# Optimization experiments

Hardware: AMD Instinct MI355X
Metric: run time of the kernel (lower is better)

Reference implementation:

```python
import jax, jax.numpy as jnp
import numpy as np

VOCAB = 32000
HID = 1024
LAYERS = 6
HEADS = 8 * 2  # 16
HEAD_DIM = HID // HEADS
INTER = int(HID * 8 / 3)  # 2730, matches torch int(hidden*8/3)
MAX_POS = 2048
EPS = 1e-5


def setup_inputs() -> dict:
    key = jax.random.key(0)
    ks = jax.random.split(key, 16)
    B, S = 2, 1024
    input_ids = jax.random.randint(ks[0], (B, S), 0, VOCAB)

    def lin(k, out_d, in_d, stack=True):
        shape = (LAYERS, out_d, in_d) if stack else (out_d, in_d)
        return jax.random.normal(k, shape, jnp.float32) * (in_d ** -0.5)

    return {
        "input_ids": input_ids,
        "tok_emb": jax.random.normal(ks[1], (VOCAB, HID), jnp.float32) * 0.02,
        "pos_emb": jax.random.normal(ks[2], (MAX_POS, HID), jnp.float32) * 0.02,
        "qkv_w": lin(ks[3], 3 * HID, HID),
        "o_w": lin(ks[4], HID, HID),
        "gate_w": lin(ks[5], INTER, HID),
        "up_w": lin(ks[6], INTER, HID),
        "down_w": lin(ks[7], HID, INTER),
        "ln1_w": jnp.ones((LAYERS, HID), jnp.float32),
        "ln1_b": jnp.zeros((LAYERS, HID), jnp.float32),
        "ln2_w": jnp.ones((LAYERS, HID), jnp.float32),
        "ln2_b": jnp.zeros((LAYERS, HID), jnp.float32),
        "lnf_w": jnp.ones((HID,), jnp.float32),
        "lnf_b": jnp.zeros((HID,), jnp.float32),
        "head_w": lin(ks[8], VOCAB, HID, stack=False),
    }


def _layernorm(x, w, b):
    mu = jnp.mean(x, axis=-1, keepdims=True)
    var = jnp.mean(jnp.square(x - mu), axis=-1, keepdims=True)
    return (x - mu) * jax.lax.rsqrt(var + EPS) * w + b


def _forward(input_ids, tok_emb, pos_emb, qkv_w, o_w, gate_w, up_w, down_w,
             ln1_w, ln1_b, ln2_w, ln2_b, lnf_w, lnf_b, head_w):
    B, S = input_ids.shape
    h = tok_emb[input_ids] + pos_emb[jnp.arange(S)][None, :, :]  # [B,S,H]
    scale = HEAD_DIM ** -0.5

    def layer(h, p):
        qkv_w, o_w, gate_w, up_w, down_w, l1w, l1b, l2w, l2b = p
        # attention block
        x = _layernorm(h, l1w, l1b)
        qkv = jnp.einsum('bsh,oh->bso', x, qkv_w)  # [B,S,3H]
        qkv = qkv.reshape(B, S, 3, HEADS, HEAD_DIM)
        q, k, v = qkv[:, :, 0], qkv[:, :, 1], qkv[:, :, 2]  # [B,S,Hn,Dh]
        attn = jnp.einsum('bqnd,bknd->bnqk', q, k) * scale  # [B,Hn,S,S]
        attn = jax.nn.softmax(attn, axis=-1)
        ctx = jnp.einsum('bnqk,bknd->bqnd', attn, v).reshape(B, S, HID)
        h = h + jnp.einsum('bsh,oh->bso', ctx, o_w)
        # MLP block (SwiGLU)
        x = _layernorm(h, l2w, l2b)
        gate = jax.nn.silu(jnp.einsum('bsh,ih->bsi', x, gate_w))
        up = jnp.einsum('bsh,ih->bsi', x, up_w)
        h = h + jnp.einsum('bsi,hi->bsh', gate * up, down_w)
        return h, None

    h, _ = jax.lax.scan(layer, h, (qkv_w, o_w, gate_w, up_w, down_w,
                                   ln1_w, ln1_b, ln2_w, ln2_b))
    h = _layernorm(h, lnf_w, lnf_b)
    logits = jnp.einsum('bsh,vh->bsv', h, head_w)  # [B,S,V]
    return logits


def reference(input_ids, tok_emb, pos_emb, qkv_w, o_w, gate_w, up_w, down_w,
              ln1_w, ln1_b, ln2_w, ln2_b, lnf_w, lnf_b, head_w):
    return _forward(input_ids, tok_emb, pos_emb, qkv_w, o_w, gate_w, up_w,
                    down_w, ln1_w, ln1_b, ln2_w, ln2_b, lnf_w, lnf_b, head_w)
```

## Files before the change

### kernel.cpp

```cpp
#include <hip/hip_runtime.h>

typedef unsigned short u16;
typedef __attribute__((ext_vector_type(8))) short bf16x8;
typedef __attribute__((ext_vector_type(8))) unsigned short us8;
typedef __attribute__((ext_vector_type(4))) unsigned short us4;
typedef __attribute__((ext_vector_type(4))) float f32x4;

#define SEQ    1024
#define TOK    2048
#define HID    1024
#define NLAYER 6
#define NHEAD  16
#define HDIM   64
#define QKV3   3072
#define INTER  2730
#define IPAD   2816
#define VOCAB  32000
#define LN_EPS 1e-5f

__device__ __forceinline__ u16 f2bf(float f) {
  unsigned u = __float_as_uint(f);
  return (u16)((u + 0x7fffu + ((u >> 16) & 1u)) >> 16);
}
__device__ __forceinline__ float bf2f(u16 u) {
  return __uint_as_float(((unsigned)u) << 16);
}

__device__ __forceinline__ void gl_lds16(const void* g, void* l) {
  __builtin_amdgcn_global_load_lds(
      (const __attribute__((address_space(1))) void*)g,
      (__attribute__((address_space(3))) void*)l, 16, 0, 0);
}

__global__ __launch_bounds__(256) void embed_kernel(
    const int* __restrict__ ids, const float* __restrict__ tok,
    const float* __restrict__ pos, float* __restrict__ h)
{
  int t = blockIdx.x;
  int s = t & (SEQ - 1);
  int id = ids[t];
  int c = threadIdx.x * 4;
  float4 tv = *(const float4*)(tok + (long)id * HID + c);
  float4 pv = *(const float4*)(pos + (long)s * HID + c);
  float4 o;
  o.x = tv.x + pv.x; o.y = tv.y + pv.y; o.z = tv.z + pv.z; o.w = tv.w + pv.w;
  *(float4*)(h + (long)t * HID + c) = o;
}

__device__ __forceinline__ void ln_body(
    int t, int tid, const float* __restrict__ h, const float* __restrict__ w,
    const float* __restrict__ b, u16* __restrict__ out, float* r1, float* r2)
{
  int lane = tid & 63, wid = tid >> 6;
  float4 v = *(const float4*)(h + (long)t * HID + tid * 4);
  float s1 = v.x + v.y + v.z + v.w;
  float s2 = v.x * v.x + v.y * v.y + v.z * v.z + v.w * v.w;
#pragma unroll
  for (int o = 32; o > 0; o >>= 1) { s1 += __shfl_down(s1, o); s2 += __shfl_down(s2, o); }
  if (lane == 0) { r1[wid] = s1; r2[wid] = s2; }
  __syncthreads();
  float t1 = r1[0] + r1[1] + r1[2] + r1[3];
  float t2 = r2[0] + r2[1] + r2[2] + r2[3];
  float mu = t1 * (1.f / HID);
  float var = t2 * (1.f / HID) - mu * mu;
  float rs = rsqrtf(var + LN_EPS);
  float4 wv = *(const float4*)(w + tid * 4);
  float4 bv = *(const float4*)(b + tid * 4);
  us4 o4;
  o4[0] = f2bf((v.x - mu) * rs * wv.x + bv.x);
  o4[1] = f2bf((v.y - mu) * rs * wv.y + bv.y);
  o4[2] = f2bf((v.z - mu) * rs * wv.z + bv.z);
  o4[3] = f2bf((v.w - mu) * rs * wv.w + bv.w);
  *(us4*)(out + (long)t * HID + tid * 4) = o4;
}

__global__ __launch_bounds__(256) void ln_kernel(
    const float* __restrict__ h, const float* __restrict__ w,
    const float* __restrict__ b, u16* __restrict__ out)
{
  __shared__ float r1[4], r2[4];
  ln_body(blockIdx.x, threadIdx.x, h, w, b, out, r1, r2);
}

__global__ __launch_bounds__(256) void pre_kernel(
    const float* __restrict__ h, const float* __restrict__ lw,
    const float* __restrict__ lb, u16* __restrict__ x,
    const float* __restrict__ qkv_w, const float* __restrict__ o_w,
    const float* __restrict__ gate, const float* __restrict__ up,
    const float* __restrict__ down,
    u16* __restrict__ wq, u16* __restrict__ wo,
    u16* __restrict__ wgu, u16* __restrict__ wd)
{
  __shared__ float r1[4], r2[4];
  int bid = blockIdx.x;
  if (bid < 2048) {
    ln_body(bid, threadIdx.x, h, lw, lb, x, r1, r2);
    return;
  }
  long i = (long)(bid - 2048) * 256 + threadIdx.x;
  us8 o;
  if (i < 393216L) {
    const float* s = qkv_w + i * 8;
#pragma unroll
    for (int j = 0; j < 8; ++j) o[j] = f2bf(s[j]);
    *(us8*)(wq + i * 8) = o;
  } else if (i < 524288L) {
    long i2 = i - 393216L;
    const float* s = o_w + i2 * 8;
#pragma unroll
    for (int j = 0; j < 8; ++j) o[j] = f2bf(s[j]);
    *(us8*)(wo + i2 * 8) = o;
  } else if (i < 1245184L) {
    long i3 = i - 524288L;
    int n = (int)(i3 >> 7);
    int kc = (int)(i3 & 127);
    int g = n >> 1;
    const float* s = (n & 1) ? up : gate;
#pragma unroll
    for (int j = 0; j < 8; ++j) {
      int k = kc * 8 + j;
      o[j] = f2bf((g < INTER) ? s[(long)g * HID + k] : 0.f);
    }
    *(us8*)(wgu + i3 * 8) = o;
  } else {
    long i4 = i - 1245184L;
    int n = (int)(i4 / 352);
    int kc = (int)(i4 % 352);
#pragma unroll
    for (int j = 0; j < 8; ++j) {
      int k = kc * 8 + j;
      o[j] = f2bf((k < INTER) ? down[(long)n * INTER + k] : 0.f);
    }
    *(us8*)(wd + i4 * 8) = o;
  }
}

__global__ __launch_bounds__(256) void fin_kernel(
    const float* __restrict__ h, const float* __restrict__ lw,
    const float* __restrict__ lb, u16* __restrict__ x,
    const float* __restrict__ head_w, u16* __restrict__ whead)
{
  __shared__ float r1[4], r2[4];
  int bid = blockIdx.x;
  if (bid < 2048) {
    ln_body(bid, threadIdx.x, h, lw, lb, x, r1, r2);
    return;
  }
  long i = (long)(bid - 2048) * 256 + threadIdx.x;
  const float* s = head_w + i * 8;
  us8 o;
#pragma unroll
  for (int j = 0; j < 8; ++j) o[j] = f2bf(s[j]);
  *(us8*)(whead + i * 8) = o;
}

__global__ __launch_bounds__(256, 3) void attn_kernel(
    const u16* __restrict__ qkv, const u16* __restrict__ vT,
    u16* __restrict__ ctx)
{
  __shared__ u16 Ks[8][128][8];
  __shared__ u16 Vs[16][64][8];
  __shared__ u16 Ps[4][16 * 128];

  const int tid  = threadIdx.x;
  const int lane = tid & 63;
  const int w    = tid >> 6;
  const int lo   = lane & 15;
  const int hi   = lane >> 4;

  const int z  = blockIdx.x & 31;
  const int qt = blockIdx.x >> 5;
  const int b  = z >> 4, h = z & 15;

  const u16* Qb  = qkv + (long)b * SEQ * QKV3 + h * 64;
  const u16* Kb  = Qb + 1024;
  const u16* Vtb = vT + (long)z * 65536;

  bf16x8 q[2];
#pragma unroll
  for (int ks = 0; ks < 2; ++ks)
    q[ks] = *(const bf16x8*)(Qb + (long)(qt * 64 + w * 16 + lo) * QKV3 + ks * 32 + hi * 8);

  f32x4 po[4];
  float m_run[4], l_run[4];
#pragma unroll
  for (int r = 0; r < 4; ++r) { m_run[r] = -1e30f; l_run[r] = 0.f; }
#pragma unroll
  for (int nd = 0; nd < 4; ++nd) po[nd] = (f32x4){0.f, 0.f, 0.f, 0.f};

  char* Pw = (char*)&Ps[w][0];

  for (int c = 0; c < 8; ++c) {
#pragma unroll
    for (int i = 0; i < 4; ++i) {
      int u = w * 4 + i, g = u & 7, rg = u >> 3;
      gl_lds16(Kb + (long)(c * 128 + rg * 64 + lane) * QKV3 + g * 8, &Ks[g][rg * 64][0]);
    }
#pragma unroll
    for (int i = 0; i < 4; ++i) {
      int kg = w * 4 + i;
      gl_lds16(Vtb + (long)lane * 1024 + c * 128 + kg * 8, &Vs[kg][0][0]);
    }
    __syncthreads();

    f32x4 s[8];
#pragma unroll
    for (int jf = 0; jf < 8; ++jf) s[jf] = (f32x4){0.f, 0.f, 0.f, 0.f};
#pragma unroll
    for (int jf = 0; jf < 8; ++jf) {
      bf16x8 bk[2];
#pragma unroll
      for (int ks = 0; ks < 2; ++ks)
        bk[ks] = *(const bf16x8*)&Ks[ks * 4 + hi][jf * 16 + lo][0];
#pragma unroll
      for (int ks = 0; ks < 2; ++ks)
        s[jf] = __builtin_amdgcn_mfma_f32_16x16x32_bf16(q[ks], bk[ks], s[jf], 0, 0, 0);
    }

    float scf[4];
#pragma unroll
    for (int r = 0; r < 4; ++r) {
      float rm = -1e30f;
#pragma unroll
      for (int jf = 0; jf < 8; ++jf) {
        s[jf][r] *= 0.125f;
        rm = fmaxf(rm, s[jf][r]);
      }
#pragma unroll
      for (int o = 1; o < 16; o <<= 1) rm = fmaxf(rm, __shfl_xor(rm, o));
      float mn = fmaxf(m_run[r], rm);
      float sc = __expf(m_run[r] - mn);
      float rs = 0.f;
#pragma unroll
      for (int jf = 0; jf < 8; ++jf) {
        float e = __expf(s[jf][r] - mn);
        s[jf][r] = e;
        rs += e;
      }
#pragma unroll
      for (int o = 1; o < 16; o <<= 1) rs += __shfl_xor(rs, o);
      l_run[r] = l_run[r] * sc + rs;
      m_run[r] = mn;
      scf[r] = sc;
    }

#pragma unroll
    for (int jf = 0; jf < 8; ++jf)
#pragma unroll
      for (int r = 0; r < 4; ++r) {
        int row = hi * 4 + r;
        int byo = row * 256 + ((((jf * 16 + lo) * 2)) ^ ((row & 7) << 4));
        *(u16*)(Pw + byo) = f2bf(s[jf][r]);
      }
#pragma unroll
    for (int nd = 0; nd < 4; ++nd)
#pragma unroll
      for (int r = 0; r < 4; ++r) po[nd][r] *= scf[r];

    bf16x8 pa[4];
#pragma unroll
    for (int ks2 = 0; ks2 < 4; ++ks2) {
      int row = lo;
      int byo = row * 256 + (((ks2 * 32 + hi * 8) * 2) ^ ((row & 7) << 4));
      pa[ks2] = *(const bf16x8*)(Pw + byo);
    }
#pragma unroll
    for (int nd = 0; nd < 4; ++nd) {
      bf16x8 bv[4];
#pragma unroll
      for (int ks2 = 0; ks2 < 4; ++ks2)
        bv[ks2] = *(const bf16x8*)&Vs[ks2 * 4 + hi][nd * 16 + lo][0];
#pragma unroll
      for (int ks2 = 0; ks2 < 4; ++ks2)
        po[nd] = __builtin_amdgcn_mfma_f32_16x16x32_bf16(pa[ks2], bv[ks2], po[nd], 0, 0, 0);
    }
    __syncthreads();
  }

#pragma unroll
  for (int r = 0; r < 4; ++r) {
    float inv = 1.f / l_run[r];
    int qrow = qt * 64 + w * 16 + hi * 4 + r;
    u16* dst = ctx + (long)(b * SEQ + qrow) * HID + h * 64;
#pragma unroll
    for (int nd = 0; nd < 4; ++nd)
      dst[nd * 16 + lo] = f2bf(po[nd][r] * inv);
  }
}

template<int BM, int BN, int EPI>
__global__ __launch_bounds__(256) void gemm_bt(
    const u16* __restrict__ A, const u16* __restrict__ B,
    void* __restrict__ Cv, const float* __restrict__ resid,
    int lda, int ldb, int ldc, int K, float scale, int bdiv,
    long sA1, long sA2, long sB1, long sB2, long sC1, long sC2)
{
  constexpr int FM = BM / 32;
  constexpr int FN = BN / 32;
  constexpr int TRW = 136;
  constexpr int SMEMU = (EPI == 4 && 128 * TRW > 2 * (BM + BN) * 32)
                        ? 128 * TRW : 2 * (BM + BN) * 32;
  __shared__ u16 smem[SMEMU];
  auto absb = [&](int buf) { return smem + buf * (BM * 32); };
  auto bsb  = [&](int buf) { return smem + 2 * (BM * 32) + buf * (BN * 32); };

  const int tid = threadIdx.x;
  const int lane = tid & 63;
  const int wid = tid >> 6;
  const int wm = wid >> 1, wn = wid & 1;

  const int z = blockIdx.z;
  const long offA = (long)(z / bdiv) * sA1 + (long)(z % bdiv) * sA2;
  const long offB = (long)(z / bdiv) * sB1 + (long)(z % bdiv) * sB2;
  const long offC = (long)(z / bdiv) * sC1 + (long)(z % bdiv) * sC2;

  const u16* Ab = A + offA + (long)blockIdx.x * BM * lda;
  const u16* Bb = B + offB + (long)blockIdx.y * BN * ldb;

  auto stage = [&](int buf, int kt) {
    const u16* a = Ab + (long)kt * 32;
    const u16* bsrc = Bb + (long)kt * 32;
#pragma unroll
    for (int i = 0; i < BM / 64; ++i) {
      int row = i * 64 + wid * 16 + (lane >> 2);
      gl_lds16(a + (long)row * lda + (lane & 3) * 8, absb(buf) + i * 2048 + wid * 512);
    }
#pragma unroll
    for (int i = 0; i < BN / 64; ++i) {
      int row = i * 64 + wid * 16 + (lane >> 2);
      gl_lds16(bsrc + (long)row * ldb + (lane & 3) * 8, bsb(buf) + i * 2048 + wid * 512);
    }
  };

  f32x4 acc[FM][FN];
#pragma unroll
  for (int i = 0; i < FM; ++i)
#pragma unroll
    for (int j = 0; j < FN; ++j) acc[i][j] = (f32x4){0.f, 0.f, 0.f, 0.f};

  int aoff[FM], boff[FN];
#pragma unroll
  for (int i = 0; i < FM; ++i)
    aoff[i] = (wm * (BM / 2) + i * 16 + (lane & 15)) * 32 + (lane >> 4) * 8;
#pragma unroll
  for (int j = 0; j < FN; ++j)
    boff[j] = (wn * (BN / 2) + j * 16 + (lane & 15)) * 32 + (lane >> 4) * 8;

  const int KT = K >> 5;
  stage(0, 0);
  __syncthreads();
  int cur = 0;
  for (int kt = 0; kt < KT; ++kt) {
    if (kt + 1 < KT) stage(cur ^ 1, kt + 1);
    bf16x8 av[FM], bv[FN];
#pragma unroll
    for (int i = 0; i < FM; ++i) av[i] = *(const bf16x8*)(absb(cur) + aoff[i]);
#pragma unroll
    for (int j = 0; j < FN; ++j) bv[j] = *(const bf16x8*)(bsb(cur) + boff[j]);
#pragma unroll
    for (int i = 0; i < FM; ++i)
#pragma unroll
      for (int j = 0; j < FN; ++j)
        acc[i][j] = __builtin_amdgcn_mfma_f32_16x16x32_bf16(av[i], bv[j], acc[i][j], 0, 0, 0);
    __syncthreads();
    cur ^= 1;
  }

  const int r0 = blockIdx.x * BM + wm * (BM / 2) + (lane >> 4) * 4;
  const int c0 = blockIdx.y * BN + wn * (BN / 2) + (lane & 15);

  if (EPI == 4 && blockIdx.y >= 16) {
    u16* Tr = smem;
    const int clb = wn * 64 + (lane & 15);
    const int rlb = wm * 64 + (lane >> 4) * 4;
#pragma unroll
    for (int i = 0; i < FM; ++i) {
#pragma unroll
      for (int j = 0; j < FN; ++j) {
        us4 t4;
#pragma unroll
        for (int r = 0; r < 4; ++r) t4[r] = f2bf(acc[i][j][r]);
        *(us4*)(Tr + (clb + j * 16) * TRW + rlb + i * 16) = t4;
      }
    }
    __syncthreads();
    const int bb  = blockIdx.x >> 3;
    const int k0  = (blockIdx.x & 7) * 128;
    const int vcb = blockIdx.y * 128 - 2048;
    const int c_loc = tid >> 1, half = tid & 1;
    const int vcol = vcb + c_loc;
    u16* vTo = (u16*)(void*)resid;
    u16* dst = vTo + (long)(bb * 16 + (vcol >> 6)) * 65536
             + (long)(vcol & 63) * 1024 + k0 + half * 64;
    const u16* srcl = Tr + c_loc * TRW + half * 64;
#pragma unroll
    for (int j = 0; j < 8; ++j)
      *(us8*)(dst + j * 8) = *(const us8*)(srcl + j * 8);
    return;
  }

#pragma unroll
  for (int i = 0; i < FM; ++i) {
#pragma unroll
    for (int j = 0; j < FN; ++j) {
      f32x4 v = acc[i][j];
#pragma unroll
      for (int r = 0; r < 4; ++r) {
        if (EPI == 3) {
          float pv = __shfl_xor(v[r], 1);
          if ((lane & 1) == 0) {
            float gf = v[r];
            float res = gf / (1.f + __expf(-gf)) * pv;
            int cc = c0 + j * 16;
            long idx = offC + (long)(r0 + i * 16 + r) * ldc + (cc >> 1);
            ((u16*)Cv)[idx] = f2bf(res);
          }
        } else {
          long idx = offC + (long)(r0 + i * 16 + r) * ldc + (c0 + j * 16);
          if (EPI == 0 || EPI == 4) ((u16*)Cv)[idx] = f2bf(v[r] * scale);
          else if (EPI == 1)        ((float*)Cv)[idx] = v[r] * scale;
          else                      ((float*)Cv)[idx] = resid[idx] + v[r];
        }
      }
    }
  }
}

template<int EPI>
__global__ __launch_bounds__(512, 1) void gemm256(
    const u16* __restrict__ A, const u16* __restrict__ B,
    void* __restrict__ Cv, int NB, int ldc)
{
  __shared__ u16 lds[2][2][2][8][128][8];

  const int tid  = threadIdx.x;
  const int lane = tid & 63;
  const int w    = tid >> 6;
  const int wm   = w >> 2;
  const int wn   = w & 3;
  const int arow = lane & 15;
  const int kg   = lane >> 4;

  const int flat = blockIdx.x;
  const int swz  = (flat & 7) * NB + (flat >> 3);
  const int bm   = swz & 7;
  const int bn   = swz >> 3;

  const u16* Ab = A + (long)bm * 256 * 1024;
  const u16* Bb = B + (long)bn * 256 * 1024;

  auto stage = [&](int mat, int d, int half, int t) {
#pragma unroll
    for (int i = 0; i < 2; ++i) {
      const int u  = w * 2 + i;
      const int g  = u & 7;
      const int rg = u >> 3;
      const u16* src = (mat == 0 ? Ab : Bb)
                     + (long)(half * 128 + rg * 64 + lane) * 1024 + t * 64 + g * 8;
      gl_lds16(src, &lds[d][mat][half][g][rg * 64][0]);
    }
  };

  f32x4 acc[2][2][4][2];
#pragma unroll
  for (int qm = 0; qm < 2; ++qm)
#pragma unroll
    for (int qn = 0; qn < 2; ++qn)
#pragma unroll
      for (int f = 0; f < 4; ++f)
#pragma unroll
        for (int n = 0; n < 2; ++n) acc[qm][qn][f][n] = (f32x4){0.f, 0.f, 0.f, 0.f};

  bf16x8 a[4][2];
  bf16x8 b[2][2][2];

  auto rdA = [&](int d, int qm) {
#pragma unroll
    for (int f = 0; f < 4; ++f)
#pragma unroll
      for (int ks = 0; ks < 2; ++ks)
        a[f][ks] = *(const bf16x8*)&lds[d][0][wm][ks * 4 + kg][qm * 64 + f * 16 + arow][0];
  };
  auto rdB = [&](int d, int qn) {
#pragma unroll
    for (int n = 0; n < 2; ++n)
#pragma unroll
      for (int ks = 0; ks < 2; ++ks)
        b[qn][n][ks] = *(const bf16x8*)&lds[d][1][wn >> 1][ks * 4 + kg]
                                          [(wn & 1) * 64 + qn * 32 + n * 16 + arow][0];
  };
  auto mm = [&](int qm, int qn) {
#pragma unroll
    for (int f = 0; f < 4; ++f)
#pragma unroll
      for (int n = 0; n < 2; ++n)
#pragma unroll
        for (int ks = 0; ks < 2; ++ks)
          acc[qm][qn][f][n] = __builtin_amdgcn_mfma_f32_16x16x32_bf16(
              a[f][ks], b[qn][n][ks], acc[qm][qn][f][n], 0, 0, 0);
  };

#define BAR asm volatile("s_barrier" ::: "memory")
#define PRIO1 __builtin_amdgcn_s_setprio(1)
#define PRIO0 __builtin_amdgcn_s_setprio(0)

  stage(1, 0, 0, 0);
  stage(0, 0, 0, 0);
  stage(0, 0, 1, 0);
  stage(1, 0, 1, 0);
  stage(1, 1, 0, 1);
  stage(0, 1, 0, 1);
  asm volatile("s_waitcnt vmcnt(4)" ::: "memory");
  BAR;

  const int iters = 8;
#pragma unroll 1
  for (int it = 0; it < iters; ++it) {
    const int T = 2 * it;
    const bool pf = (it + 1 < iters);
    rdA(0, 0); rdB(0, 0); rdB(0, 1);
    stage(0, 1, 1, T + 1);
    stage(1, 1, 1, T + 1);
    BAR; PRIO1; mm(0, 0); mm(0, 1); PRIO0; BAR;
    rdA(0, 1);
    if (pf) { stage(1, 0, 0, T + 2);
              stage(0, 0, 0, T + 2); }
    BAR; PRIO1; mm(1, 0); mm(1, 1); PRIO0;
    if (pf) asm volatile("s_waitcnt vmcnt(4)" ::: "memory");
    else    asm volatile("s_waitcnt vmcnt(0)" ::: "memory");
    BAR;
    rdA(1, 0); rdB(1, 0); rdB(1, 1);
    if (pf) { stage(0, 0, 1, T + 2);
              stage(1, 0, 1, T + 2); }
    BAR; PRIO1; mm(0, 0); mm(0, 1); PRIO0; BAR;
    rdA(1, 1);
    if (pf) { stage(1, 1, 0, T + 3);
              stage(0, 1, 0, T + 3); }
    BAR; PRIO1; mm(1, 0); mm(1, 1); PRIO0;
    if (pf) asm volatile("s_waitcnt vmcnt(4)" ::: "memory");
    BAR;
  }
#undef BAR
#undef PRIO1
#undef PRIO0

#pragma unroll
  for (int qm = 0; qm < 2; ++qm) {
#pragma unroll
    for (int qn = 0; qn < 2; ++qn) {
#pragma unroll
      for (int f = 0; f < 4; ++f) {
        const int r0 = bm * 256 + wm * 128 + qm * 64 + f * 16 + kg * 4;
#pragma unroll
        for (int n = 0; n < 2; ++n) {
          const int c = bn * 256 + wn * 64 + qn * 32 + n * 16 + arow;
          f32x4 v = acc[qm][qn][f][n];
#pragma unroll
          for (int r = 0; r < 4; ++r) {
            long idx = (long)(r0 + r) * ldc + c;
            if (EPI == 0) ((u16*)Cv)[idx] = f2bf(v[r]);
            else          ((float*)Cv)[idx] = v[r];
          }
        }
      }
    }
  }
}

extern "C" void kernel_launch(void* const* d_in, const int* in_sizes, int n_in,
                              void* d_out, int out_size, void* d_ws, size_t ws_size,
                              hipStream_t stream)
{
  (void)in_sizes; (void)n_in; (void)out_size; (void)ws_size;
  const int*   ids     = (const int*)d_in[0];
  const float* tok_emb = (const float*)d_in[1];
  const float* pos_emb = (const float*)d_in[2];
  const float* qkv_w   = (const float*)d_in[3];
  const float* o_w     = (const float*)d_in[4];
  const float* gate_w  = (const float*)d_in[5];
  const float* up_w    = (const float*)d_in[6];
  const float* down_w  = (const float*)d_in[7];
  const float* ln1_w   = (const float*)d_in[8];
  const float* ln1_b   = (const float*)d_in[9];
  const float* ln2_w   = (const float*)d_in[10];
  const float* ln2_b   = (const float*)d_in[11];
  const float* lnf_w   = (const float*)d_in[12];
  const float* lnf_b   = (const float*)d_in[13];
  const float* head_w  = (const float*)d_in[14];

  char* ws = (char*)d_ws;
  long off = 0;
  auto alloc = [&](long bytes) { void* p = ws + off; off += (bytes + 1023) & ~1023L; return p; };
  float* h   = (float*)alloc((long)TOK * HID * 4);
  u16*   x   = (u16*)  alloc((long)TOK * HID * 2);
  u16*   qkv = (u16*)  alloc((long)TOK * QKV3 * 2);
  u16*   vT  = (u16*)  alloc(32L * HDIM * SEQ * 2);
  u16*   ctx = (u16*)  alloc((long)TOK * HID * 2);
  u16*   y   = (u16*)  alloc((long)TOK * IPAD * 2);
  u16*   whead = (u16*)alloc((long)VOCAB * HID * 2);
  u16* wq  = whead;
  u16* wo  = wq + 3072 * 1024;
  u16* wgu = wo + 1024 * 1024;
  u16* wd  = wgu + 5632 * 1024;

  embed_kernel<<<TOK, 256, 0, stream>>>(ids, tok_emb, pos_emb, h);

  for (int l = 0; l < NLAYER; ++l) {
    pre_kernel<<<8320, 256, 0, stream>>>(
        h, ln1_w + l * HID, ln1_b + l * HID, x,
        qkv_w + (long)l * QKV3 * HID, o_w + (long)l * HID * HID,
        gate_w + (long)l * INTER * HID, up_w + (long)l * INTER * HID,
        down_w + (long)l * HID * INTER, wq, wo, wgu, wd);

    gemm_bt<128, 128, 4><<<dim3(16, 24, 1), 256, 0, stream>>>(
        x, wq, qkv, (const float*)vT, HID, HID, QKV3, HID, 1.f, 1, 0, 0, 0, 0, 0, 0);

    attn_kernel<<<dim3(512), 256, 0, stream>>>(qkv, vT, ctx);

    gemm_bt<64, 128, 2><<<dim3(32, 8, 1), 256, 0, stream>>>(
        ctx, wo, h, h, HID, HID, HID, HID, 1.f, 1, 0, 0, 0, 0, 0, 0);

    ln_kernel<<<TOK, 256, 0, stream>>>(h, ln2_w + l * HID, ln2_b + l * HID, x);

    gemm_bt<128, 128, 3><<<dim3(16, 44, 1), 256, 0, stream>>>(
        x, wgu, y, nullptr, HID, HID, IPAD, HID, 1.f, 1, 0, 0, 0, 0, 0, 0);

    gemm_bt<64, 128, 2><<<dim3(32, 8, 1), 256, 0, stream>>>(
        y, wd, h, h, IPAD, IPAD, HID, IPAD, 1.f, 1, 0, 0, 0, 0, 0, 0);
  }

  fin_kernel<<<18048, 256, 0, stream>>>(h, lnf_w, lnf_b, x, head_w, whead);
  gemm256<1><<<dim3(1000), 512, 0, stream>>>(x, whead, d_out, 125, VOCAB);
}
```

Baseline: 1.236 ms.

## Overlap per-layer weight bf16 conversion with the attention kernel

```diff
diff --git a/kernel.cpp b/kernel.cpp
--- a/kernel.cpp
+++ b/kernel.cpp
@@ -82,14 +82,10 @@
   ln_body(blockIdx.x, threadIdx.x, h, w, b, out, r1, r2);
 }
 
-__global__ __launch_bounds__(256) void pre_kernel(
+__global__ __launch_bounds__(256) void pre1_kernel(
     const float* __restrict__ h, const float* __restrict__ lw,
     const float* __restrict__ lb, u16* __restrict__ x,
-    const float* __restrict__ qkv_w, const float* __restrict__ o_w,
-    const float* __restrict__ gate, const float* __restrict__ up,
-    const float* __restrict__ down,
-    u16* __restrict__ wq, u16* __restrict__ wo,
-    u16* __restrict__ wgu, u16* __restrict__ wd)
+    const float* __restrict__ qkv_w, u16* __restrict__ wq)
 {
   __shared__ float r1[4], r2[4];
   int bid = blockIdx.x;
@@ -98,41 +94,11 @@
     return;
   }
   long i = (long)(bid - 2048) * 256 + threadIdx.x;
+  const float* s = qkv_w + i * 8;
   us8 o;
-  if (i < 393216L) {
-    const float* s = qkv_w + i * 8;
-#pragma unroll
-    for (int j = 0; j < 8; ++j) o[j] = f2bf(s[j]);
-    *(us8*)(wq + i * 8) = o;
-  } else if (i < 524288L) {
-    long i2 = i - 393216L;
-    const float* s = o_w + i2 * 8;
-#pragma unroll
-    for (int j = 0; j < 8; ++j) o[j] = f2bf(s[j]);
-    *(us8*)(wo + i2 * 8) = o;
-  } else if (i < 1245184L) {
-    long i3 = i - 524288L;
-    int n = (int)(i3 >> 7);
-    int kc = (int)(i3 & 127);
-    int g = n >> 1;
-    const float* s = (n & 1) ? up : gate;
-#pragma unroll
-    for (int j = 0; j < 8; ++j) {
-      int k = kc * 8 + j;
-      o[j] = f2bf((g < INTER) ? s[(long)g * HID + k] : 0.f);
-    }
-    *(us8*)(wgu + i3 * 8) = o;
-  } else {
-    long i4 = i - 1245184L;
-    int n = (int)(i4 / 352);
-    int kc = (int)(i4 % 352);
-#pragma unroll
-    for (int j = 0; j < 8; ++j) {
-      int k = kc * 8 + j;
-      o[j] = f2bf((k < INTER) ? down[(long)n * INTER + k] : 0.f);
-    }
-    *(us8*)(wd + i4 * 8) = o;
-  }
+#pragma unroll
+  for (int j = 0; j < 8; ++j) o[j] = f2bf(s[j]);
+  *(us8*)(wq + i * 8) = o;
 }
 
 __global__ __launch_bounds__(256) void fin_kernel(
@@ -154,22 +120,69 @@
   *(us8*)(whead + i * 8) = o;
 }
 
-__global__ __launch_bounds__(256, 3) void attn_kernel(
+__global__ __launch_bounds__(256, 3) void attn_cvt_kernel(
     const u16* __restrict__ qkv, const u16* __restrict__ vT,
-    u16* __restrict__ ctx)
+    u16* __restrict__ ctx,
+    const float* __restrict__ o_w, const float* __restrict__ gate,
+    const float* __restrict__ up, const float* __restrict__ down,
+    const float* __restrict__ next_qkv_w,
+    u16* __restrict__ wo, u16* __restrict__ wgu, u16* __restrict__ wd,
+    u16* __restrict__ wq)
 {
   __shared__ u16 Ks[8][128][8];
   __shared__ u16 Vs[16][64][8];
   __shared__ u16 Ps[4][16 * 128];
 
-  const int tid  = threadIdx.x;
+  const int bid = blockIdx.x;
+  const int tid = threadIdx.x;
+
+  if (bid >= 512) {
+    long i = (long)(bid - 512) * 256 + tid;
+    us8 o;
+    if (i < 131072L) {
+      const float* s = o_w + i * 8;
+#pragma unroll
+      for (int j = 0; j < 8; ++j) o[j] = f2bf(s[j]);
+      *(us8*)(wo + i * 8) = o;
+    } else if (i < 851968L) {
+      long i3 = i - 131072L;
+      int n = (int)(i3 >> 7);
+      int kc = (int)(i3 & 127);
+      int g = n >> 1;
+      const float* s = (n & 1) ? up : gate;
+#pragma unroll
+      for (int j = 0; j < 8; ++j) {
+        int k = kc * 8 + j;
+        o[j] = f2bf((g < INTER) ? s[(long)g * HID + k] : 0.f);
+      }
+      *(us8*)(wgu + i3 * 8) = o;
+    } else if (i < 1212416L) {
+      long i4 = i - 851968L;
+      int n = (int)(i4 / 352);
+      int kc = (int)(i4 % 352);
+#pragma unroll
+      for (int j = 0; j < 8; ++j) {
+        int k = kc * 8 + j;
+        o[j] = f2bf((k < INTER) ? down[(long)n * INTER + k] : 0.f);
+      }
+      *(us8*)(wd + i4 * 8) = o;
+    } else {
+      long i5 = i - 1212416L;
+      const float* s = next_qkv_w + i5 * 8;
+#pragma unroll
+      for (int j = 0; j < 8; ++j) o[j] = f2bf(s[j]);
+      *(us8*)(wq + i5 * 8) = o;
+    }
+    return;
+  }
+
   const int lane = tid & 63;
   const int w    = tid >> 6;
   const int lo   = lane & 15;
   const int hi   = lane >> 4;
 
-  const int z  = blockIdx.x & 31;
-  const int qt = blockIdx.x >> 5;
+  const int z  = bid & 31;
+  const int qt = bid >> 5;
   const int b  = z >> 4, h = z & 15;
 
   const u16* Qb  = qkv + (long)b * SEQ * QKV3 + h * 64;
@@ -606,16 +619,24 @@
   embed_kernel<<<TOK, 256, 0, stream>>>(ids, tok_emb, pos_emb, h);
 
   for (int l = 0; l < NLAYER; ++l) {
-    pre_kernel<<<8320, 256, 0, stream>>>(
-        h, ln1_w + l * HID, ln1_b + l * HID, x,
-        qkv_w + (long)l * QKV3 * HID, o_w + (long)l * HID * HID,
-        gate_w + (long)l * INTER * HID, up_w + (long)l * INTER * HID,
-        down_w + (long)l * HID * INTER, wq, wo, wgu, wd);
+    if (l == 0) {
+      pre1_kernel<<<3584, 256, 0, stream>>>(
+          h, ln1_w, ln1_b, x, qkv_w, wq);
+    } else {
+      ln_kernel<<<TOK, 256, 0, stream>>>(h, ln1_w + l * HID, ln1_b + l * HID, x);
+    }
 
     gemm_bt<128, 128, 4><<<dim3(16, 24, 1), 256, 0, stream>>>(
         x, wq, qkv, (const float*)vT, HID, HID, QKV3, HID, 1.f, 1, 0, 0, 0, 0, 0, 0);
 
-    attn_kernel<<<dim3(512), 256, 0, stream>>>(qkv, vT, ctx);
+    const int cvt_blocks = (l + 1 < NLAYER) ? 6272 : 4736;
+    attn_cvt_kernel<<<dim3(512 + cvt_blocks), 256, 0, stream>>>(
+        qkv, vT, ctx,
+        o_w + (long)l * HID * HID,
+        gate_w + (long)l * INTER * HID, up_w + (long)l * INTER * HID,
+        down_w + (long)l * HID * INTER,
+        qkv_w + (long)(l + 1 < NLAYER ? l + 1 : l) * QKV3 * HID,
+        wo, wgu, wd, wq);
 
     gemm_bt<64, 128, 2><<<dim3(32, 8, 1), 256, 0, stream>>>(
         ctx, wo, h, h, HID, HID, HID, HID, 1.f, 1, 0, 0, 0, 0, 0, 0);
```

New measurement: 1.206 ms (median of 2 runs). -2.5%, faster.
